# Kernel tuning notes

Measured on AMD Instinct MI355X. Metric: run time of the kernel, lower is better.

## Reference

```python
import jax, jax.numpy as jnp
import numpy as np

EPS = 1e-5

def _layer_norm(x, g, b):
    mu = jnp.mean(x, axis=-1, keepdims=True)
    var = jnp.mean(jnp.square(x - mu), axis=-1, keepdims=True)
    return (x - mu) * jax.lax.rsqrt(var + EPS) * g + b

def setup_inputs() -> dict:
    key = jax.random.key(0)
    ks = jax.random.split(key, 8)
    B, S, H, NH, FF = 2, 2048, 2048, 16, 8192
    x = jax.random.normal(ks[0], (B, S, H), dtype=jnp.float32)
    # causal mask: True = masked (matches masked_fill semantics)
    mask = jnp.triu(jnp.ones((S, S), dtype=bool), k=1)
    sc = 0.02
    wq = jax.random.normal(ks[1], (H, H), dtype=jnp.float32) * sc
    wk = jax.random.normal(ks[2], (H, H), dtype=jnp.float32) * sc
    wv = jax.random.normal(ks[3], (H, H), dtype=jnp.float32) * sc
    wo = jax.random.normal(ks[4], (H, H), dtype=jnp.float32) * sc
    w_in = jax.random.normal(ks[5], (H, FF), dtype=jnp.float32) * sc
    w_out = jax.random.normal(ks[6], (FF, H), dtype=jnp.float32) * sc
    ln1_g = jnp.ones((H,), jnp.float32); ln1_b = jnp.zeros((H,), jnp.float32)
    ln2_g = jnp.ones((H,), jnp.float32); ln2_b = jnp.zeros((H,), jnp.float32)
    return {"x": x, "mask": mask, "wq": wq, "wk": wk, "wv": wv, "wo": wo,
            "w_in": w_in, "w_out": w_out,
            "ln1_g": ln1_g, "ln1_b": ln1_b, "ln2_g": ln2_g, "ln2_b": ln2_b}

def reference(x, mask, wq, wk, wv, wo, w_in, w_out, ln1_g, ln1_b, ln2_g, ln2_b):
    B, S, H = x.shape
    NH = 16
    HD = H // NH
    scale = HD ** (-0.5)
    # attention with pre-norm
    xn = _layer_norm(x, ln1_g, ln1_b)
    q = (xn @ wq).reshape(B, S, NH, HD)
    k = (xn @ wk).reshape(B, S, NH, HD)
    v = (xn @ wv).reshape(B, S, NH, HD)
    scores = jnp.einsum('bqhd,bkhd->bhqk', q, k) * scale
    scores = jnp.where(mask[:S, :S], -jnp.inf, scores)
    attn = jax.nn.softmax(scores, axis=-1)
    out = jnp.einsum('bhqk,bkhd->bqhd', attn, v).reshape(B, S, H)
    h = x + out @ wo
    # FFN with pre-norm, tanh-approx GELU
    hn = _layer_norm(h, ln2_g, ln2_b)
    ff = jax.nn.gelu(hn @ w_in, approximate=True) @ w_out
    return h + ff
```

## Files before the change

### kernel.cpp

```cpp
#include <hip/hip_runtime.h>
#include <hip/hip_bf16.h>

#define B_ 2
#define S_ 2048
#define H_ 2048
#define NH_ 16
#define HD_ 128
#define FF_ 8192

typedef __attribute__((ext_vector_type(8))) short bf16x8;
typedef __attribute__((ext_vector_type(4))) float f32x4;

#define NEG_BIG (-1e30f)

#define GLL16(gp, lp)                                                                    \
  __builtin_amdgcn_global_load_lds((const __attribute__((address_space(1))) void*)(gp),  \
                                   (__attribute__((address_space(3))) void*)(lp), 16, 0, 0)

__device__ __forceinline__ float b2f(unsigned short u) {
  union { unsigned int i; float f; } c; c.i = ((unsigned int)u) << 16; return c.f;
}
__device__ __forceinline__ unsigned short f2b(float f) {
  unsigned int u = __float_as_uint(f);
  u += 0x7fffu + ((u >> 16) & 1u);
  return (unsigned short)(u >> 16);
}
__device__ __forceinline__ float ldf(const void* p, size_t i, int f32) {
  return f32 ? ((const float*)p)[i] : b2f(((const unsigned short*)p)[i]);
}
__device__ __forceinline__ void unpack8(uint4 r, float* f) {
  f[0] = b2f((unsigned short)(r.x & 0xffffu)); f[1] = b2f((unsigned short)(r.x >> 16));
  f[2] = b2f((unsigned short)(r.y & 0xffffu)); f[3] = b2f((unsigned short)(r.y >> 16));
  f[4] = b2f((unsigned short)(r.z & 0xffffu)); f[5] = b2f((unsigned short)(r.z >> 16));
  f[6] = b2f((unsigned short)(r.w & 0xffffu)); f[7] = b2f((unsigned short)(r.w >> 16));
}

__global__ void detect_k(const unsigned int* __restrict__ x, int* __restrict__ flagp) {
  if (threadIdx.x == 0) {
    int c = 0;
    for (int i = 0; i < 256; ++i) {
      unsigned int e = (x[i] >> 7) & 0xffu;
      c += (e >= 97u && e <= 130u) ? 1 : 0;
    }
    *flagp = (c < 128) ? 1 : 0;
  }
}

__global__ __launch_bounds__(256) void transpose_k(const void* __restrict__ in,
                                                   unsigned short* __restrict__ out,
                                                   int R, int C,
                                                   const int* __restrict__ flagp) {
  __shared__ unsigned short tile[32][33];
  int f32 = *flagp;
  int r0 = blockIdx.y * 32, c0 = blockIdx.x * 32;
  int tx = threadIdx.x & 31, ty = threadIdx.x >> 5;
#pragma unroll
  for (int p = 0; p < 4; ++p)
    tile[ty + p * 8][tx] = f2b(ldf(in, (size_t)(r0 + ty + p * 8) * C + c0 + tx, f32));
  __syncthreads();
#pragma unroll
  for (int p = 0; p < 4; ++p)
    out[(size_t)(c0 + ty + p * 8) * R + r0 + tx] = tile[tx][ty + p * 8];
}

__global__ __launch_bounds__(256) void v_transpose_k(const unsigned short* __restrict__ qkv,
                                                     unsigned short* __restrict__ VT) {
  __shared__ unsigned short tile[32][33];
  int bh = blockIdx.z;
  int b = bh >> 4, h = bh & 15;
  int s0 = blockIdx.x * 32, d0 = blockIdx.y * 32;
  int tx = threadIdx.x & 31, ty = threadIdx.x >> 5;
#pragma unroll
  for (int p = 0; p < 4; ++p) {
    int s = s0 + ty + p * 8;
    tile[ty + p * 8][tx] = qkv[(size_t)(b * S_ + s) * (3 * H_) + 2 * H_ + h * HD_ + d0 + tx];
  }
  __syncthreads();
#pragma unroll
  for (int p = 0; p < 4; ++p)
    VT[((size_t)bh * HD_ + d0 + ty + p * 8) * S_ + s0 + tx] = tile[tx][ty + p * 8];
}

__global__ __launch_bounds__(256) void ln_k(const void* __restrict__ x,
                                            const void* __restrict__ g,
                                            const void* __restrict__ b,
                                            unsigned short* __restrict__ y,
                                            const int* __restrict__ flagp, int in_mode) {
  __shared__ float red[2][4];
  int f32 = *flagp;
  int xf = in_mode ? f32 : 0;
  int row = blockIdx.x;
  int t = threadIdx.x;
  float v[8];
  size_t base = (size_t)row * H_ + t * 8;
  if (xf) {
    const float4* p = reinterpret_cast<const float4*>((const float*)x + base);
    float4 u0 = p[0], u1 = p[1];
    v[0] = u0.x; v[1] = u0.y; v[2] = u0.z; v[3] = u0.w;
    v[4] = u1.x; v[5] = u1.y; v[6] = u1.z; v[7] = u1.w;
  } else {
    unpack8(*reinterpret_cast<const uint4*>((const unsigned short*)x + base), v);
  }
  float s1 = 0.f, s2 = 0.f;
#pragma unroll
  for (int i = 0; i < 8; ++i) { s1 += v[i]; s2 += v[i] * v[i]; }
#pragma unroll
  for (int off = 32; off > 0; off >>= 1) {
    s1 += __shfl_down(s1, off);
    s2 += __shfl_down(s2, off);
  }
  int w = t >> 6, lane = t & 63;
  if (lane == 0) { red[0][w] = s1; red[1][w] = s2; }
  __syncthreads();
  s1 = red[0][0] + red[0][1] + red[0][2] + red[0][3];
  s2 = red[1][0] + red[1][1] + red[1][2] + red[1][3];
  float mu = s1 * (1.0f / H_);
  float var = s2 * (1.0f / H_) - mu * mu;
  float rinv = rsqrtf(var + 1e-5f);
  float gv[8], bv[8];
#pragma unroll
  for (int i = 0; i < 8; ++i) {
    gv[i] = ldf(g, t * 8 + i, f32);
    bv[i] = ldf(b, t * 8 + i, f32);
  }
  unsigned int o[4];
#pragma unroll
  for (int i = 0; i < 4; ++i) {
    unsigned short lo = f2b((v[2 * i] - mu) * rinv * gv[2 * i] + bv[2 * i]);
    unsigned short hi = f2b((v[2 * i + 1] - mu) * rinv * gv[2 * i + 1] + bv[2 * i + 1]);
    o[i] = (unsigned int)lo | ((unsigned int)hi << 16);
  }
  uint4 ov; ov.x = o[0]; ov.y = o[1]; ov.z = o[2]; ov.w = o[3];
  *reinterpret_cast<uint4*>(y + base) = ov;
}

#define PH_BAR() do { asm volatile("" ::: "memory"); __builtin_amdgcn_s_barrier(); \
                      asm volatile("" ::: "memory"); } while (0)
#define VMC(n) asm volatile("s_waitcnt vmcnt(" #n ")" ::: "memory")

#define STA(buf_, h_, kt_) do {                                                        \
  GLL16(pA0 + (size_t)(h_) * 128 * K + (kt_) * 64, &LdsA[buf_][(h_) * 8192 + lw]);     \
  GLL16(pA1 + (size_t)(h_) * 128 * K + (kt_) * 64, &LdsA[buf_][(h_) * 8192 + 4096 + lw]); } while (0)
#define STB(buf_, h_, kt_) do {                                                        \
  GLL16(pB0 + (size_t)(h_) * 128 * K + (kt_) * 64, &LdsB[buf_][(h_) * 8192 + lw]);     \
  GLL16(pB1 + (size_t)(h_) * 128 * K + (kt_) * 64, &LdsB[buf_][(h_) * 8192 + 4096 + lw]); } while (0)

#define LDA4(AF, buf_, mb_) do { _Pragma("unroll")                                     \
  for (int mi_ = 0; mi_ < 4; ++mi_) {                                                  \
    const unsigned short* _p = &LdsA[buf_][(wr * 128 + ((mb_) + mi_) * 16 + l15) * 64];\
    AF[mi_][0] = *reinterpret_cast<const bf16x8*>(_p + cs0);                           \
    AF[mi_][1] = *reinterpret_cast<const bf16x8*>(_p + cs1); } } while (0)
#define LDB2(BF, buf_, nb_) do { _Pragma("unroll")                                     \
  for (int ni_ = 0; ni_ < 2; ++ni_) {                                                  \
    const unsigned short* _p = &LdsB[buf_][(wc * 64 + ((nb_) + ni_) * 16 + l15) * 64]; \
    BF[ni_][0] = *reinterpret_cast<const bf16x8*>(_p + cs0);                           \
    BF[ni_][1] = *reinterpret_cast<const bf16x8*>(_p + cs1); } } while (0)

#define MF8(AF, BF, MO, NO) do { _Pragma("unroll")                                     \
  for (int h_ = 0; h_ < 2; ++h_) { _Pragma("unroll")                                   \
    for (int mi_ = 0; mi_ < 4; ++mi_) { _Pragma("unroll")                              \
      for (int ni_ = 0; ni_ < 2; ++ni_) {                                              \
        acc[(MO) + mi_][(NO) + ni_] = __builtin_amdgcn_mfma_f32_16x16x32_bf16(         \
            AF[mi_][h_], BF[ni_][h_], acc[(MO) + mi_][(NO) + ni_], 0, 0, 0);           \
      } } } } while (0)

#define PH_MFMA(AF, BF, MO, NO) do {                                                   \
  PH_BAR(); __builtin_amdgcn_s_setprio(1);                                             \
  MF8(AF, BF, MO, NO);                                                                 \
  __builtin_amdgcn_s_setprio(0); } while (0)

#define GITER(LAST, tO, tE2, tO2) do {                                                 \
                                                                              \
  LDA4(aL, 0, 0); LDB2(bL, 0, 0);                                                      \
  STA(1, 1, tO);                                                                       \
  PH_MFMA(aL, bL, 0, 0);                                                               \
                                                                              \
  LDB2(bH, 0, 2);                                                                      \
  PH_MFMA(aL, bH, 0, 2);                                                               \
                                                                              \
  LDA4(aH, 0, 4);                                                                      \
  if (!(LAST)) STB(0, 0, tE2);                                                         \
  PH_MFMA(aH, bL, 4, 0);                                                               \
                                                                              \
  if (!(LAST)) { STB(0, 1, tE2); STA(0, 0, tE2); VMC(6); } else { VMC(0); }            \
  PH_MFMA(aH, bH, 4, 2);                                                               \
                                                                              \
  LDA4(aL, 1, 0); LDB2(bL, 1, 0);                                                      \
  if (!(LAST)) STA(0, 1, tE2);                                                         \
  PH_MFMA(aL, bL, 0, 0);                                                               \
                                                                              \
  LDB2(bH, 1, 2);                                                                      \
  PH_MFMA(aL, bH, 0, 2);                                                               \
                                                                              \
  LDA4(aH, 1, 4);                                                                      \
  if (!(LAST)) STB(1, 0, tO2);                                                         \
  PH_MFMA(aH, bL, 4, 0);                                                               \
                                                                              \
  if (!(LAST)) { STB(1, 1, tO2); STA(1, 0, tO2); VMC(6); }                             \
  PH_MFMA(aH, bH, 4, 2);                                                               \
} while (0)

template <int EPI>
__global__ __launch_bounds__(512) void gemm256(const unsigned short* __restrict__ A,
                                               const unsigned short* __restrict__ BT,
                                               void* __restrict__ C,
                                               const void* __restrict__ resid,
                                               int M, int N, int K,
                                               const int* __restrict__ flagp,
                                               int resid_mode, int store_mode, int nbx,
                                               int nxy, int Klen,
                                               size_t pslice, int prow) {
  (void)M;
  __shared__ unsigned short LdsA[2][16384];
  __shared__ unsigned short LdsB[2][16384];

  unsigned nwg = gridDim.x, q = nwg >> 3;
  unsigned o = blockIdx.x;
  unsigned wg = (o & 7u) * q + (o >> 3);
  int ks = 0;
  if (nxy) { ks = (int)(wg / (unsigned)nxy); wg -= (unsigned)ks * (unsigned)nxy; }
  int bx = (int)((wg >> 3) % (unsigned)nbx);
  int by = (int)((wg >> 3) / (unsigned)nbx) * 8 + (int)(wg & 7u);
  int m_base = by * 256, n_base = bx * 256;
  size_t koff = (size_t)ks * (size_t)Klen;

  int tid = threadIdx.x;
  int w = tid >> 6, lane = tid & 63;
  int l15 = lane & 15, quad = lane >> 4;
  int wr = w >> 2, wc = w & 3;

  int row0 = w * 8 + (lane >> 3);
  int scb  = (lane & 7) ^ (lane >> 3);
  const unsigned short* pA0 = A + (size_t)(m_base + row0) * K + koff + scb * 8;
  const unsigned short* pA1 = pA0 + (size_t)64 * K;
  const unsigned short* pB0 = BT + (size_t)(n_base + row0) * K + koff + scb * 8;
  const unsigned short* pB1 = pB0 + (size_t)64 * K;
  unsigned lw = (unsigned)w * 512;

  int cs0 = ((quad) ^ (l15 & 7)) * 8;
  int cs1 = ((4 + quad) ^ (l15 & 7)) * 8;

  f32x4 acc[8][4];
#pragma unroll
  for (int i = 0; i < 8; ++i)
#pragma unroll
    for (int j = 0; j < 4; ++j) acc[i][j] = (f32x4){0.f, 0.f, 0.f, 0.f};

  bf16x8 aL[4][2], aH[4][2], bL[2][2], bH[2][2];

  STA(0, 0, 0); STA(0, 1, 0); STB(0, 0, 0); STB(0, 1, 0);
  STB(1, 0, 1); STB(1, 1, 1); STA(1, 0, 1);
  VMC(6);
  PH_BAR();

  int niter = Klen >> 7;
  for (int i = 0; i < niter - 1; ++i) GITER(0, 2 * i + 1, 2 * i + 2, 2 * i + 3);
  GITER(1, 2 * niter - 1, 0, 0);

  int f32 = 0, rf = 0, sf = 0;
  if (EPI != 3) {
    f32 = *flagp;
    rf = resid_mode ? f32 : 0;
    sf = store_mode ? f32 : 0;
  }
#pragma unroll
  for (int mi = 0; mi < 8; ++mi) {
#pragma unroll
    for (int ni = 0; ni < 4; ++ni) {
#pragma unroll
      for (int r = 0; r < 4; ++r) {
        int row = m_base + wr * 128 + mi * 16 + quad * 4 + r;
        int col = n_base + wc * 64 + ni * 16 + l15;
        float v = acc[mi][ni][r];
        if (EPI == 3) {
          ((float*)C)[(size_t)ks * pslice + (size_t)row * prow + col] = v;
        } else {
          size_t idx = (size_t)row * N + col;
          if (EPI == 1) v += ldf(resid, idx, rf);
          if (EPI == 2) {
            float u = v;
            float tt = 0.7978845608028654f * (u + 0.044715f * u * u * u);
            tt = fminf(tt, 15.0f);
            float s = __expf(2.0f * tt);
            v = u * s / (s + 1.0f);
          }
          if (sf) ((float*)C)[idx] = v;
          else    ((unsigned short*)C)[idx] = f2b(v);
        }
      }
    }
  }
}

__global__ __launch_bounds__(256) void red_k(const float* __restrict__ P,
                                             void* __restrict__ out,
                                             const void* __restrict__ resid,
                                             int prow, size_t pslice,
                                             const int* __restrict__ flagp,
                                             int resid_mode, int store_mode) {
  int f32 = *flagp;
  int rf = resid_mode ? f32 : 0;
  int sf = store_mode ? f32 : 0;
  size_t gid = (size_t)blockIdx.x * 256 + threadIdx.x;
  int r = (int)(gid >> 8);
  int c = ((int)gid & 255) * 8;
  size_t pb = (size_t)r * prow + c;
  const float4* p0 = reinterpret_cast<const float4*>(P + pb);
  const float4* p1 = reinterpret_cast<const float4*>(P + pslice + pb);
  float4 a0 = p0[0], a1 = p0[1];
  float4 b0 = p1[0], b1 = p1[1];
  float v[8] = {a0.x + b0.x, a0.y + b0.y, a0.z + b0.z, a0.w + b0.w,
                a1.x + b1.x, a1.y + b1.y, a1.z + b1.z, a1.w + b1.w};
  size_t ob = (size_t)r * 2048 + c;
  if (rf) {
    const float4* rp = reinterpret_cast<const float4*>((const float*)resid + ob);
    float4 r0 = rp[0], r1 = rp[1];
    v[0] += r0.x; v[1] += r0.y; v[2] += r0.z; v[3] += r0.w;
    v[4] += r1.x; v[5] += r1.y; v[6] += r1.z; v[7] += r1.w;
  } else {
    float rr[8];
    unpack8(*reinterpret_cast<const uint4*>((const unsigned short*)resid + ob), rr);
#pragma unroll
    for (int j = 0; j < 8; ++j) v[j] += rr[j];
  }
  if (sf) {
    float4 s0 = {v[0], v[1], v[2], v[3]}, s1 = {v[4], v[5], v[6], v[7]};
    float4* op = reinterpret_cast<float4*>((float*)out + ob);
    op[0] = s0; op[1] = s1;
  } else {
    unsigned int oo[4];
#pragma unroll
    for (int i = 0; i < 4; ++i)
      oo[i] = (unsigned int)f2b(v[2 * i]) | ((unsigned int)f2b(v[2 * i + 1]) << 16);
    uint4 ov; ov.x = oo[0]; ov.y = oo[1]; ov.z = oo[2]; ov.w = oo[3];
    *reinterpret_cast<uint4*>((unsigned short*)out + ob) = ov;
  }
}

__global__ __launch_bounds__(256) void attn_k(const unsigned short* __restrict__ qkv,
                                              const unsigned short* __restrict__ VT,
                                              unsigned short* __restrict__ out) {
  __shared__ unsigned short Ks[2][64 * 128];
  __shared__ unsigned short Vs[2][128 * 64];
  __shared__ unsigned short Ps[4][16][72];
  unsigned o = blockIdx.x;
  int xcd = (int)(o & 7u), j = (int)(o >> 3);
  int bh = xcd + 8 * (j >> 5);
  int qb = 31 - (j & 31);
  int b = bh >> 4, h = bh & 15;
  int q0 = qb * 64;
  int tid = threadIdx.x;
  int w = tid >> 6, lane = tid & 63, l15 = lane & 15, quad = lane >> 4;
  const float scale = 0.08838834764831845f;

  bf16x8 aq[4];
  {
    const unsigned short* qrow =
        qkv + (size_t)(b * S_ + q0 + w * 16 + l15) * (3 * H_) + h * HD_;
#pragma unroll
    for (int ks = 0; ks < 4; ++ks)
      aq[ks] = *reinterpret_cast<const bf16x8*>(qrow + ks * 32 + quad * 8);
  }

  int krow_off = lane >> 4;
  int kcb = lane & 15;
  int vrow_off = lane >> 3;
  int vcb = lane & 7;

  f32x4 o_[8];
#pragma unroll
  for (int f = 0; f < 8; ++f) o_[f] = (f32x4){0.f, 0.f, 0.f, 0.f};
  float m_i[4], l_i[4];
#pragma unroll
  for (int r = 0; r < 4; ++r) { m_i[r] = NEG_BIG; l_i[r] = 0.f; }

  const unsigned short* kbase = qkv + (size_t)b * S_ * (3 * H_) + H_ + h * HD_;
  const unsigned short* vbase = VT + (size_t)bh * HD_ * S_;

#define ATTN_STAGE(buf_, kv0_) do {                                                     \
  _Pragma("unroll")                                                                     \
  for (int t = 0; t < 4; ++t) {                                                         \
    int krow = w * 16 + t * 4 + krow_off;                                               \
    int ksz = kcb ^ (krow & 7);                                                         \
    GLL16(kbase + (size_t)((kv0_) + krow) * (3 * H_) + ksz * 8,                         \
          &Ks[buf_][(w * 16 + t * 4) * 128]);                                           \
    int vrow = w * 32 + t * 8 + vrow_off;                                               \
    int vsz = vcb ^ (vrow & 7);                                                         \
    GLL16(vbase + (size_t)vrow * S_ + (kv0_) + vsz * 8,                                 \
          &Vs[buf_][(w * 32 + t * 8) * 64]);                                            \
  } } while (0)

  ATTN_STAGE(0, 0);
  __syncthreads();

  int cur = 0;
  for (int kv0 = 0; kv0 <= q0; kv0 += 64, cur ^= 1) {
    if (kv0 + 64 <= q0) ATTN_STAGE(cur ^ 1, kv0 + 64);

    f32x4 sc[4];
#pragma unroll
    for (int jj = 0; jj < 4; ++jj) sc[jj] = (f32x4){0.f, 0.f, 0.f, 0.f};
#pragma unroll
    for (int ks = 0; ks < 4; ++ks) {
#pragma unroll
      for (int jj = 0; jj < 4; ++jj) {
        int r = jj * 16 + l15;
        bf16x8 bk = *reinterpret_cast<const bf16x8*>(
            &Ks[cur][r * 128 + (((ks * 4 + quad) ^ (l15 & 7))) * 8]);
        sc[jj] = __builtin_amdgcn_mfma_f32_16x16x32_bf16(aq[ks], bk, sc[jj], 0, 0, 0);
      }
    }
    bool diag = (kv0 == q0);
#pragma unroll
    for (int jj = 0; jj < 4; ++jj)
#pragma unroll
      for (int r = 0; r < 4; ++r) {
        float s = sc[jj][r] * scale;
        if (diag && (jj * 16 + l15 > w * 16 + quad * 4 + r)) s = NEG_BIG;
        sc[jj][r] = s;
      }

    float mx[4];
#pragma unroll
    for (int r = 0; r < 4; ++r) {
      mx[r] = sc[0][r];
#pragma unroll
      for (int jj = 1; jj < 4; ++jj) mx[r] = fmaxf(mx[r], sc[jj][r]);
    }
#pragma unroll
    for (int mm = 1; mm <= 8; mm <<= 1)
#pragma unroll
      for (int r = 0; r < 4; ++r) mx[r] = fmaxf(mx[r], __shfl_xor(mx[r], mm));
    float alpha[4];
#pragma unroll
    for (int r = 0; r < 4; ++r) {
      float mn = fmaxf(m_i[r], mx[r]);
      alpha[r] = __expf(m_i[r] - mn);
      m_i[r] = mn;
    }
    float pr[4][4], rs[4] = {0.f, 0.f, 0.f, 0.f};
#pragma unroll
    for (int jj = 0; jj < 4; ++jj)
#pragma unroll
      for (int r = 0; r < 4; ++r) {
        float p = __expf(sc[jj][r] - m_i[r]);
        pr[jj][r] = p;
        rs[r] += p;
      }
#pragma unroll
    for (int mm = 1; mm <= 8; mm <<= 1)
#pragma unroll
      for (int r = 0; r < 4; ++r) rs[r] += __shfl_xor(rs[r], mm);
#pragma unroll
    for (int r = 0; r < 4; ++r) l_i[r] = l_i[r] * alpha[r] + rs[r];
#pragma unroll
    for (int f = 0; f < 8; ++f)
#pragma unroll
      for (int r = 0; r < 4; ++r) o_[f][r] *= alpha[r];

#pragma unroll
    for (int jj = 0; jj < 4; ++jj)
#pragma unroll
      for (int r = 0; r < 4; ++r)
        Ps[w][quad * 4 + r][jj * 16 + l15] = f2b(pr[jj][r]);

#pragma unroll
    for (int ks2 = 0; ks2 < 2; ++ks2) {
      bf16x8 ap = *reinterpret_cast<const bf16x8*>(&Ps[w][l15][ks2 * 32 + quad * 8]);
#pragma unroll
      for (int f = 0; f < 8; ++f) {
        int r = f * 16 + l15;
        bf16x8 bv = *reinterpret_cast<const bf16x8*>(
            &Vs[cur][r * 64 + (((ks2 * 4 + quad) ^ (l15 & 7))) * 8]);
        o_[f] = __builtin_amdgcn_mfma_f32_16x16x32_bf16(ap, bv, o_[f], 0, 0, 0);
      }
    }

    __syncthreads();
  }

  float inv[4];
#pragma unroll
  for (int r = 0; r < 4; ++r) inv[r] = 1.0f / l_i[r];
#pragma unroll
  for (int f = 0; f < 8; ++f)
#pragma unroll
    for (int r = 0; r < 4; ++r)
      out[(size_t)(b * S_ + q0 + w * 16 + quad * 4 + r) * H_ + h * HD_ + f * 16 + l15] =
          f2b(o_[f][r] * inv[r]);
}

extern "C" void kernel_launch(void* const* d_in, const int* in_sizes, int n_in,
                              void* d_out, int out_size, void* d_ws, size_t ws_size,
                              hipStream_t stream) {
  (void)in_sizes; (void)n_in; (void)out_size; (void)ws_size;
  const void* x     = d_in[0];
  const void* wq    = d_in[2];
  const void* wk    = d_in[3];
  const void* wv    = d_in[4];
  const void* wo    = d_in[5];
  const void* w_in  = d_in[6];
  const void* w_out = d_in[7];
  const void* g1    = d_in[8];
  const void* b1    = d_in[9];
  const void* g2    = d_in[10];
  const void* b2    = d_in[11];
  char* ws = (char*)d_ws;

  const size_t MB = 1024 * 1024;
  unsigned short* W  = (unsigned short*)(ws + 0 * MB);
  unsigned short* E  = (unsigned short*)(ws + 32 * MB);
  unsigned short* F  = (unsigned short*)(ws + 48 * MB);
  unsigned short* Hb = (unsigned short*)(ws + 112 * MB);
  int* flagp         = (int*)(ws + 128 * MB);

  unsigned short* wqkvT = W;
  unsigned short* xn    = E;
  unsigned short* qkv   = F;
  unsigned short* VT    = F + (size_t)B_ * S_ * 3 * H_;
  unsigned short* attnb = E;
  unsigned short* hbuf  = Hb;
  unsigned short* hn    = E;
  unsigned short* ff1   = F;
  float*          Pop   = (float*)F;

  dim3 blk(256);
  dim3 gblk(512);
  detect_k<<<1, 64, 0, stream>>>((const unsigned int*)x, flagp);
  transpose_k<<<dim3(H_ / 32, H_ / 32), blk, 0, stream>>>(wq, wqkvT, H_, H_, flagp);
  transpose_k<<<dim3(H_ / 32, H_ / 32), blk, 0, stream>>>(wk, wqkvT + (size_t)H_ * H_, H_, H_, flagp);
  transpose_k<<<dim3(H_ / 32, H_ / 32), blk, 0, stream>>>(wv, wqkvT + (size_t)2 * H_ * H_, H_, H_, flagp);
  ln_k<<<B_ * S_, blk, 0, stream>>>(x, g1, b1, xn, flagp, 1);
  gemm256<0><<<dim3((3 * H_ / 256) * (B_ * S_ / 256)), gblk, 0, stream>>>(
      xn, wqkvT, qkv, nullptr, B_ * S_, 3 * H_, H_, flagp, 0, 0, 3 * H_ / 256,
      0, H_, 0, 0);
  v_transpose_k<<<dim3(S_ / 32, HD_ / 32, B_ * NH_), blk, 0, stream>>>(qkv, VT);
  attn_k<<<dim3(S_ / 64 * B_ * NH_), blk, 0, stream>>>(qkv, VT, attnb);
  transpose_k<<<dim3(H_ / 32, H_ / 32), blk, 0, stream>>>(wo, W, H_, H_, flagp);
  gemm256<3><<<dim3(2 * (H_ / 256) * (B_ * S_ / 256)), gblk, 0, stream>>>(
      attnb, W, (void*)Pop, nullptr, B_ * S_, H_, H_, flagp, 0, 0, H_ / 256,
      (H_ / 256) * (B_ * S_ / 256), H_ / 2, (size_t)B_ * S_ * H_, H_);
  red_k<<<dim3((B_ * S_ * H_) / (256 * 8)), blk, 0, stream>>>(
      Pop, hbuf, x, H_, (size_t)B_ * S_ * H_, flagp, 1, 0);
  ln_k<<<B_ * S_, blk, 0, stream>>>(hbuf, g2, b2, hn, flagp, 0);
  transpose_k<<<dim3(FF_ / 32, H_ / 32), blk, 0, stream>>>(w_in, W, H_, FF_, flagp);
  gemm256<2><<<dim3((FF_ / 256) * (B_ * S_ / 256)), gblk, 0, stream>>>(
      hn, W, ff1, nullptr, B_ * S_, FF_, H_, flagp, 0, 0, FF_ / 256,
      0, H_, 0, 0);
  transpose_k<<<dim3(H_ / 32, FF_ / 32), blk, 0, stream>>>(w_out, W, FF_, H_, flagp);
  gemm256<3><<<dim3(2 * (H_ / 256) * (B_ * S_ / 256)), gblk, 0, stream>>>(
      ff1, W, (void*)ff1, nullptr, B_ * S_, H_, FF_, flagp, 0, 0, H_ / 256,
      (H_ / 256) * (B_ * S_ / 256), FF_ / 2, (size_t)H_, 2 * H_);
  red_k<<<dim3((B_ * S_ * H_) / (256 * 8)), blk, 0, stream>>>(
      (const float*)ff1, d_out, hbuf, 2 * H_, (size_t)H_, flagp, 0, 1);
}
```

Before: 922.6 us.

## Enlarge attention query tile to 128 rows with 8 waves sharing KV tiles

The attention kernel now processes 128 query rows per block using 512 threads (8 waves) instead of 64 rows with 4 waves, so each staged K/V tile is reused by twice as many waves and total K/V global traffic halves. Causal masking is generalized to per-wave diagonal offsets, and the loop runs to q0/64+2 tiles. The P scratch buffer is changed to an XOR-swizzled layout to reduce LDS bank conflicts. Trade-offs: half as many blocks (512) and extra masked work on the last two tiles for the early waves.

```diff
diff --git a/kernel.cpp b/kernel.cpp
--- a/kernel.cpp
+++ b/kernel.cpp
@@ -337,18 +337,18 @@
   }
 }
 
-__global__ __launch_bounds__(256) void attn_k(const unsigned short* __restrict__ qkv,
+__global__ __launch_bounds__(512) void attn_k(const unsigned short* __restrict__ qkv,
                                               const unsigned short* __restrict__ VT,
                                               unsigned short* __restrict__ out) {
   __shared__ unsigned short Ks[2][64 * 128];
   __shared__ unsigned short Vs[2][128 * 64];
-  __shared__ unsigned short Ps[4][16][72];
+  __shared__ unsigned short Ps[8][16 * 64];
   unsigned o = blockIdx.x;
   int xcd = (int)(o & 7u), j = (int)(o >> 3);
-  int bh = xcd + 8 * (j >> 5);
-  int qb = 31 - (j & 31);
+  int bh = xcd + 8 * (j >> 4);
+  int qb = 15 - (j & 15);
   int b = bh >> 4, h = bh & 15;
-  int q0 = qb * 64;
+  int q0 = qb * 128;
   int tid = threadIdx.x;
   int w = tid >> 6, lane = tid & 63, l15 = lane & 15, quad = lane >> 4;
   const float scale = 0.08838834764831845f;
@@ -362,11 +362,6 @@
       aq[ks] = *reinterpret_cast<const bf16x8*>(qrow + ks * 32 + quad * 8);
   }
 
-  int krow_off = lane >> 4;
-  int kcb = lane & 15;
-  int vrow_off = lane >> 3;
-  int vcb = lane & 7;
-
   f32x4 o_[8];
 #pragma unroll
   for (int f = 0; f < 8; ++f) o_[f] = (f32x4){0.f, 0.f, 0.f, 0.f};
@@ -379,23 +374,25 @@
 
 #define ATTN_STAGE(buf_, kv0_) do {                                                     \
   _Pragma("unroll")                                                                     \
-  for (int t = 0; t < 4; ++t) {                                                         \
-    int krow = w * 16 + t * 4 + krow_off;                                               \
-    int ksz = kcb ^ (krow & 7);                                                         \
+  for (int t = 0; t < 2; ++t) {                                                         \
+    int krow = w * 8 + t * 4 + (lane >> 4);                                             \
+    int ksz = (lane & 15) ^ (krow & 7);                                                 \
     GLL16(kbase + (size_t)((kv0_) + krow) * (3 * H_) + ksz * 8,                         \
-          &Ks[buf_][(w * 16 + t * 4) * 128]);                                           \
-    int vrow = w * 32 + t * 8 + vrow_off;                                               \
-    int vsz = vcb ^ (vrow & 7);                                                         \
+          &Ks[buf_][(w * 8 + t * 4) * 128]);                                            \
+    int vrow = w * 16 + t * 8 + (lane >> 3);                                            \
+    int vsz = (lane & 7) ^ (vrow & 7);                                                  \
     GLL16(vbase + (size_t)vrow * S_ + (kv0_) + vsz * 8,                                 \
-          &Vs[buf_][(w * 32 + t * 8) * 64]);                                            \
+          &Vs[buf_][(w * 16 + t * 8) * 64]);                                            \
   } } while (0)
 
   ATTN_STAGE(0, 0);
   __syncthreads();
 
+  int nt = (q0 >> 6) + 2;
   int cur = 0;
-  for (int kv0 = 0; kv0 <= q0; kv0 += 64, cur ^= 1) {
-    if (kv0 + 64 <= q0) ATTN_STAGE(cur ^ 1, kv0 + 64);
+  for (int it = 0; it < nt; ++it, cur ^= 1) {
+    int kv0 = it * 64;
+    if (it + 1 < nt) ATTN_STAGE(cur ^ 1, kv0 + 64);
 
     f32x4 sc[4];
 #pragma unroll
@@ -410,13 +407,14 @@
         sc[jj] = __builtin_amdgcn_mfma_f32_16x16x32_bf16(aq[ks], bk, sc[jj], 0, 0, 0);
       }
     }
-    bool diag = (kv0 == q0);
+    int coff = kv0 - q0 - w * 16;
+    bool needmask = (coff + 63 > 0);
 #pragma unroll
     for (int jj = 0; jj < 4; ++jj)
 #pragma unroll
       for (int r = 0; r < 4; ++r) {
         float s = sc[jj][r] * scale;
-        if (diag && (jj * 16 + l15 > w * 16 + quad * 4 + r)) s = NEG_BIG;
+        if (needmask && (jj * 16 + l15 + coff > quad * 4 + r)) s = NEG_BIG;
         sc[jj][r] = s;
       }
 
@@ -461,12 +459,16 @@
 #pragma unroll
     for (int jj = 0; jj < 4; ++jj)
 #pragma unroll
-      for (int r = 0; r < 4; ++r)
-        Ps[w][quad * 4 + r][jj * 16 + l15] = f2b(pr[jj][r]);
+      for (int r = 0; r < 4; ++r) {
+        int prow_ = quad * 4 + r;
+        int cb = jj * 2 + (l15 >> 3);
+        Ps[w][prow_ * 64 + ((cb ^ (prow_ & 7)) * 8) + (l15 & 7)] = f2b(pr[jj][r]);
+      }
 
 #pragma unroll
     for (int ks2 = 0; ks2 < 2; ++ks2) {
-      bf16x8 ap = *reinterpret_cast<const bf16x8*>(&Ps[w][l15][ks2 * 32 + quad * 8]);
+      bf16x8 ap = *reinterpret_cast<const bf16x8*>(
+          &Ps[w][l15 * 64 + (((ks2 * 4 + quad) ^ (l15 & 7))) * 8]);
 #pragma unroll
       for (int f = 0; f < 8; ++f) {
         int r = f * 16 + l15;
@@ -535,7 +537,7 @@
       xn, wqkvT, qkv, nullptr, B_ * S_, 3 * H_, H_, flagp, 0, 0, 3 * H_ / 256,
       0, H_, 0, 0);
   v_transpose_k<<<dim3(S_ / 32, HD_ / 32, B_ * NH_), blk, 0, stream>>>(qkv, VT);
-  attn_k<<<dim3(S_ / 64 * B_ * NH_), blk, 0, stream>>>(qkv, VT, attnb);
+  attn_k<<<dim3(S_ / 128 * B_ * NH_), dim3(512), 0, stream>>>(qkv, VT, attnb);
   transpose_k<<<dim3(H_ / 32, H_ / 32), blk, 0, stream>>>(wo, W, H_, H_, flagp);
   gemm256<3><<<dim3(2 * (H_ / 256) * (B_ * S_ / 256)), gblk, 0, stream>>>(
       attnb, W, (void*)Pop, nullptr, B_ * S_, H_, H_, flagp, 0, 0, H_ / 256,
```

After: 1.017 ms. 1.1x slower.
